# Performance work log

Hardware: AMD Instinct MI355X
Metric: run time of the kernel (lower is better)

Reference implementation:

```python
import jax, jax.numpy as jnp
import numpy as np

B, L, V, D = 512, 41, 4, 64        # batch, seq_len=41 (hard-coded in source), vocab=DNA, d_model=64
NL, DI, N, DTR, K = 3, 128, 16, 4, 4  # n_layer, d_inner=2*D, d_state, dt_rank=ceil(D/16), d_conv
NS = 3  # three parallel stacks (layers1/2/3)


def setup_inputs() -> dict:
    key = jax.random.key(0)
    ks = jax.random.split(key, 16)
    s = 0.02
    nrm = lambda k, sh: jax.random.normal(k, sh, jnp.float32) * s
    A_log = jnp.log(jnp.arange(1, N + 1, dtype=jnp.float32))  # S4D-real init
    return {
        "input_ids": jax.random.randint(ks[0], (B, L), 0, V),
        "embedding": nrm(ks[1], (V, D)),
        # per-stack, per-layer Mamba block params, stacked [NS, NL, ...]
        "in_proj": nrm(ks[2], (NS, NL, D, 2 * DI)),
        "conv_w": nrm(ks[3], (NS, NL, DI, 1, K)),
        "conv_b": jnp.zeros((NS, NL, DI), jnp.float32),
        "x_proj": nrm(ks[4], (NS, NL, DI, DTR + 2 * N)),
        "dt_w": nrm(ks[5], (NS, NL, DTR, DI)),
        "dt_b": jnp.full((NS, NL, DI), -2.0, jnp.float32),
        "A_log": jnp.broadcast_to(A_log, (NS, NL, DI, N)) + 0.0,
        "Dp": jnp.ones((NS, NL, DI), jnp.float32),
        "out_proj": nrm(ks[6], (NS, NL, DI, D)),
        "norm_w": jnp.ones((NS, NL, D), jnp.float32),
        "norm_f_w": jnp.ones((D,), jnp.float32),
        "fusion_w": jnp.zeros((NS,), jnp.float32),  # softmax-weighted fusion of the 3 representations
        # LastDense MLP head: 64*41 -> 384 -> 16 -> 1 (dropout is eval-mode identity)
        "W1": nrm(ks[7], (D * L, 384)), "b1": jnp.zeros((384,), jnp.float32),
        "W2": nrm(ks[8], (384, 16)), "b2": jnp.zeros((16,), jnp.float32),
        "W3": nrm(ks[9], (16, 1)), "b3": jnp.zeros((1,), jnp.float32),
    }


def rmsnorm(x, w, eps=1e-5):
    return x * jax.lax.rsqrt(jnp.mean(x * x, axis=-1, keepdims=True) + eps) * w


def silu(x):
    return x * jax.nn.sigmoid(x)


def mamba_block(x, ip, cw, cb, xp, dw, db, al, dp, op):
    # x: [B, L, D]
    bsz = x.shape[0]
    u, res = jnp.split(x @ ip, 2, axis=-1)  # each [B, L, DI]
    # causal depthwise conv1d (torch padding=3 then [..., :L] == left-pad K-1)
    uc = jax.lax.conv_general_dilated(
        u.transpose(0, 2, 1), cw, window_strides=(1,), padding=[(K - 1, 0)],
        feature_group_count=DI, dimension_numbers=("NCH", "OIH", "NCH"))
    u = silu((uc + cb[None, :, None]).transpose(0, 2, 1))  # [B, L, DI]
    dbl = u @ xp  # [B, L, DTR+2N]
    dt = jax.nn.softplus(dbl[..., :DTR] @ dw + db)           # [B, L, DI]
    Bm = dbl[..., DTR:DTR + N]                               # [B, L, N]
    C = dbl[..., DTR + N:]                                   # [B, L, N]
    A = -jnp.exp(al)                                         # [DI, N]
    dA = jnp.exp(dt[..., None] * A)                          # [B, L, DI, N]
    dBu = dt[..., None] * Bm[:, :, None, :] * u[..., None]   # [B, L, DI, N]

    def step(h, xs):
        dA_t, dBu_t, C_t = xs
        h = dA_t * h + dBu_t                                 # [B, DI, N]
        return h, jnp.einsum("bdn,bn->bd", h, C_t)

    h0 = jnp.zeros((bsz, DI, N), x.dtype)
    _, ys = jax.lax.scan(step, h0, (dA.transpose(1, 0, 2, 3), dBu.transpose(1, 0, 2, 3), C.transpose(1, 0, 2)))
    y = ys.transpose(1, 0, 2) + u * dp                       # [B, L, DI]
    return (y * silu(res)) @ op                              # [B, L, D]


def _forward(input_ids, embedding, in_proj, conv_w, conv_b, x_proj, dt_w, dt_b,
             A_log, Dp, out_proj, norm_w, norm_f_w, fusion_w, W1, b1, W2, b2, W3, b3):
    emb = embedding[input_ids]  # [B, L, D]

    def run_stack(ip, cw, cb, xp, dw, db, al, dp, op, nw):
        x = emb
        for i in range(NL):  # residual: x + MambaBlock(RMSNorm(x))
            x = x + mamba_block(rmsnorm(x, nw[i]), ip[i], cw[i], cb[i], xp[i], dw[i], db[i], al[i], dp[i], op[i])
        return x

    stack_out = jax.vmap(run_stack)(in_proj, conv_w, conv_b, x_proj, dt_w, dt_b,
                                    A_log, Dp, out_proj, norm_w)  # [NS, B, L, D]
    stack_out = rmsnorm(stack_out, norm_f_w)  # final norm_f per stack
    fused = jnp.einsum("s,sbld->bld", jax.nn.softmax(fusion_w), stack_out)  # fusion of 3 reps
    flat = fused.reshape(fused.shape[0], L * D)
    h = jax.nn.relu(flat @ W1 + b1)
    h = jax.nn.relu(h @ W2 + b2)
    logits = (h @ W3 + b3)[:, 0]
    return jax.nn.sigmoid(logits)  # [B]


def reference(input_ids, embedding, in_proj, conv_w, conv_b, x_proj, dt_w, dt_b,
              A_log, Dp, out_proj, norm_w, norm_f_w, fusion_w, W1, b1, W2, b2, W3, b3):
    return _forward(input_ids, embedding, in_proj, conv_w, conv_b, x_proj, dt_w, dt_b,
                    A_log, Dp, out_proj, norm_w, norm_f_w, fusion_w, W1, b1, W2, b2, W3, b3)
```

## Files before the change

kernel.cpp:

```cpp
#include <hip/hip_runtime.h>
#include <hip/hip_bf16.h>
#include <math.h>

#define Bq  512
#define Lq  41
#define Vq  4
#define Dq  64
#define NLq 3
#define DIq 128
#define Nq  16
#define DTRq 4
#define Kq  4
#define NSq 3
#define H1q 384
#define H2q 16
#define FLATq (Lq*Dq)

typedef __attribute__((ext_vector_type(8))) short frag8;
typedef __attribute__((ext_vector_type(4))) float f32x4;

__device__ __forceinline__ float b2f(unsigned short u) {
    union { float f; unsigned int i; } v; v.i = ((unsigned int)u) << 16; return v.f;
}
__device__ __forceinline__ unsigned short f2b(float f) {
    union { float f; unsigned int i; } v; v.f = f;
    unsigned int x = v.i;
    unsigned int r = (x + 0x7fffu + ((x >> 16) & 1u)) >> 16;
    return (unsigned short)r;
}

__global__ __launch_bounds__(256) void init_kernel(const int* __restrict__ ids,
                                                   const float* __restrict__ emb,
                                                   float* __restrict__ X) {
    int idx = blockIdx.x * 256 + threadIdx.x;
    const int total = NSq * Bq * Lq * Dq;
    if (idx < total) {
        int d  = idx & (Dq - 1);
        int t  = idx >> 6;
        int bl = t % (Bq * Lq);
        int id = ids[bl];
        X[idx] = emb[id * Dq + d];
    }
}

__global__ __launch_bounds__(256) void prep_small(const float* __restrict__ in_proj,
                                                  const float* __restrict__ x_proj,
                                                  const float* __restrict__ out_proj,
                                                  unsigned short* __restrict__ Wb_in,
                                                  unsigned short* __restrict__ xp_b,
                                                  unsigned short* __restrict__ op_b) {
    int idx = blockIdx.x * 256 + threadIdx.x;
    if (idx < 9*256*64) {
        int sl = idx >> 14, rem = idx & 16383;
        int n = rem >> 6, k = rem & 63;
        Wb_in[idx] = f2b(in_proj[(size_t)sl*16384 + k*256 + n]);
    } else if (idx < 9*256*64 + 9*48*128) {
        int i2 = idx - 9*256*64;
        int sl = i2 / 6144, rem = i2 % 6144;
        int c = rem >> 7, k = rem & 127;
        float v = (c < 36) ? x_proj[(size_t)sl*(128*36) + k*36 + c] : 0.f;
        xp_b[i2] = f2b(v);
    } else if (idx < 9*256*64 + 9*48*128 + 9*64*128) {
        int i3 = idx - (9*256*64 + 9*48*128);
        int sl = i3 >> 13, rem = i3 & 8191;
        int n = rem >> 7, k = rem & 127;
        op_b[i3] = f2b(out_proj[(size_t)sl*8192 + k*64 + n]);
    }
}

__global__ __launch_bounds__(256) void transpose_w1(const float* __restrict__ W1,
                                                    unsigned short* __restrict__ W1b) {
    __shared__ float t[64][65];
    const int k0 = blockIdx.x * 64, n0 = blockIdx.y * 64;
    for (int idx = threadIdx.x; idx < 4096; idx += 256) {
        int kr = idx >> 6, nc = idx & 63;
        t[kr][nc] = W1[(size_t)(k0 + kr) * H1q + n0 + nc];
    }
    __syncthreads();
    for (int idx = threadIdx.x; idx < 4096; idx += 256) {
        int nr = idx >> 6, kc = idx & 63;
        W1b[(size_t)(n0 + nr) * FLATq + k0 + kc] = f2b(t[kc][nr]);
    }
}

__global__ __launch_bounds__(256, 4) void layer_kernel(
    float* __restrict__ X,
    const unsigned short* __restrict__ Wb_in,
    const float* __restrict__ conv_w,
    const float* __restrict__ conv_b,
    const unsigned short* __restrict__ xp_b,
    const float* __restrict__ dt_w,
    const float* __restrict__ dt_b,
    const float* __restrict__ A_log,
    const float* __restrict__ Dp,
    const unsigned short* __restrict__ op_b,
    const float* __restrict__ norm_w,
    int layer)
{
    const int b = blockIdx.x, s = blockIdx.y, tid = threadIdx.x;
    const int sl = s * NLq + layer;
    const int wave = tid >> 6, lane = tid & 63;
    const int nl = lane & 15, quad = lane >> 4;

    __shared__ unsigned short xn_lb[48][72];
    __shared__ unsigned short u_lb [48][136];
    __shared__ unsigned short rs_lb[41][136];
    __shared__ float dbl_s[41][48];

    float* xrow = X + ((size_t)(s * Bq + b)) * (Lq * Dq);

    {
        const float nwv = norm_w[(size_t)sl * Dq + lane];
        for (int l = wave; l < 48; l += 4) {
            if (l < Lq) {
                float v  = xrow[l * Dq + lane];
                float ss = v * v;
                #pragma unroll
                for (int off = 32; off; off >>= 1) ss += __shfl_xor(ss, off, 64);
                float scale = rsqrtf(ss * (1.0f / Dq) + 1e-5f);
                xn_lb[l][lane] = f2b(v * scale * nwv);
            } else {
                xn_lb[l][lane] = 0;
            }
        }
    }
    __syncthreads();

    {
        #pragma unroll
        for (int t = 0; t < 12; ++t) {
            const int id = wave * 12 + t;
            const int mt = id >> 4, nt = id & 15;
            const unsigned short* Wp = Wb_in + ((size_t)(sl * 256 + nt * 16 + nl)) * 64 + quad * 8;
            frag8 a0 = *(const frag8*)&xn_lb[mt * 16 + nl][quad * 8];
            frag8 a1 = *(const frag8*)&xn_lb[mt * 16 + nl][32 + quad * 8];
            frag8 b0 = *(const frag8*)&Wp[0];
            frag8 b1 = *(const frag8*)&Wp[32];
            f32x4 c = {0.f, 0.f, 0.f, 0.f};
            c = __builtin_amdgcn_mfma_f32_16x16x32_bf16(a0, b0, c, 0, 0, 0);
            c = __builtin_amdgcn_mfma_f32_16x16x32_bf16(a1, b1, c, 0, 0, 0);
            const int col = nt * 16 + nl;
            const int r0 = mt * 16 + quad * 4;
            if (col < DIq) {
                #pragma unroll
                for (int r = 0; r < 4; ++r) u_lb[r0 + r][col] = f2b(c[r]);
            } else {
                const int d = col - DIq;
                #pragma unroll
                for (int r = 0; r < 4; ++r) {
                    int row = r0 + r;
                    if (row < Lq) {
                        float v = c[r];
                        rs_lb[row][d] = f2b(v / (1.f + __expf(-v)));
                    }
                }
            }
        }
    }
    __syncthreads();

    {
        const float* cw = conv_w + (size_t)sl * (DIq * Kq);
        const int d = tid >> 1, half = tid & 1;
        const float c0 = cw[d*4+0], c1 = cw[d*4+1], c2 = cw[d*4+2], c3 = cw[d*4+3];
        const float cbv = conv_b[(size_t)sl * DIq + d];
        float w0 = 0.f, w1 = 0.f, w2 = 0.f;
        if (half) { w0 = b2f(u_lb[18][d]); w1 = b2f(u_lb[19][d]); w2 = b2f(u_lb[20][d]); }
        const int base = half ? 21 : 0;
        const int cnt  = half ? 20 : 21;
        for (int i = 0; i < cnt; ++i) {
            int l = base + i;
            float cur = b2f(u_lb[l][d]);
            float a = fmaf(w0, c0, fmaf(w1, c1, fmaf(w2, c2, fmaf(cur, c3, cbv))));
            u_lb[l][d] = f2b(a / (1.f + __expf(-a)));
            w0 = w1; w1 = w2; w2 = cur;
        }
    }
    __syncthreads();

    {
        for (int t = wave; t < 9; t += 4) {
            const int mt = t / 3, ct = t % 3;
            f32x4 c = {0.f, 0.f, 0.f, 0.f};
            #pragma unroll
            for (int kt = 0; kt < 4; ++kt) {
                frag8 a  = *(const frag8*)&u_lb[mt * 16 + nl][kt * 32 + quad * 8];
                frag8 bb = *(const frag8*)&xp_b[((size_t)(sl * 48 + ct * 16 + nl)) * 128 + kt * 32 + quad * 8];
                c = __builtin_amdgcn_mfma_f32_16x16x32_bf16(a, bb, c, 0, 0, 0);
            }
            const int col = ct * 16 + nl, r0 = mt * 16 + quad * 4;
            #pragma unroll
            for (int r = 0; r < 4; ++r) {
                int row = r0 + r;
                if (row < Lq) dbl_s[row][col] = c[r];
            }
        }
    }
    __syncthreads();

    {
        const int d = tid >> 1, half = tid & 1;
        const float* al = A_log + (size_t)sl * (DIq * Nq) + d * Nq + half * 8;
        float A[8], h[8];
        #pragma unroll
        for (int n = 0; n < 8; ++n) { A[n] = -__expf(al[n]); h[n] = 0.f; }
        const float* dw = dt_w + (size_t)sl * (DTRq * DIq);
        const float dw0 = dw[d], dw1 = dw[DIq + d], dw2 = dw[2*DIq + d], dw3 = dw[3*DIq + d];
        const float dbv = dt_b[(size_t)sl * DIq + d];
        const float dpd = Dp[(size_t)sl * DIq + d];
        for (int l = 0; l < Lq; ++l) {
            float4 q0 = *(const float4*)&dbl_s[l][0];
            float x  = fmaf(q0.x, dw0, fmaf(q0.y, dw1, fmaf(q0.z, dw2, fmaf(q0.w, dw3, dbv))));
            float dt_ = fmaxf(x, 0.f) + __logf(1.f + __expf(-fabsf(x)));
            float u_  = b2f(u_lb[l][d]);
            float rsv = b2f(rs_lb[l][d]);
            float4 B0 = *(const float4*)&dbl_s[l][4  + half * 8];
            float4 B1 = *(const float4*)&dbl_s[l][8  + half * 8];
            float4 C0 = *(const float4*)&dbl_s[l][20 + half * 8];
            float4 C1 = *(const float4*)&dbl_s[l][24 + half * 8];
            float dtu = dt_ * u_;
            float Bv[8] = {B0.x,B0.y,B0.z,B0.w,B1.x,B1.y,B1.z,B1.w};
            float Cv[8] = {C0.x,C0.y,C0.z,C0.w,C1.x,C1.y,C1.z,C1.w};
            float y = 0.f;
            #pragma unroll
            for (int n = 0; n < 8; ++n) {
                float dA = __expf(dt_ * A[n]);
                h[n] = fmaf(dA, h[n], Bv[n] * dtu);
                y    = fmaf(h[n], Cv[n], y);
            }
            y += __shfl_xor(y, 1, 64);
            if (!half) u_lb[l][d] = f2b(fmaf(u_, dpd, y) * rsv);
        }
    }
    __syncthreads();

    {
        const int ntG = wave;
        for (int mt = 0; mt < 3; ++mt) {
            f32x4 c = {0.f, 0.f, 0.f, 0.f};
            #pragma unroll
            for (int kt = 0; kt < 4; ++kt) {
                frag8 a  = *(const frag8*)&u_lb[mt * 16 + nl][kt * 32 + quad * 8];
                frag8 bb = *(const frag8*)&op_b[((size_t)(sl * 64 + ntG * 16 + nl)) * 128 + kt * 32 + quad * 8];
                c = __builtin_amdgcn_mfma_f32_16x16x32_bf16(a, bb, c, 0, 0, 0);
            }
            const int j = ntG * 16 + nl, r0 = mt * 16 + quad * 4;
            #pragma unroll
            for (int r = 0; r < 4; ++r) {
                int row = r0 + r;
                if (row < Lq) xrow[row * Dq + j] += c[r];
            }
        }
    }
}

__global__ __launch_bounds__(256) void head_fuse(const float* __restrict__ X,
                                                 const float* __restrict__ norm_f_w,
                                                 const float* __restrict__ fusion_w,
                                                 unsigned short* __restrict__ Flat_b) {
    const int b    = blockIdx.x;
    const int tid  = threadIdx.x;
    const int wave = tid >> 6, lane = tid & 63;

    float fw0 = fusion_w[0], fw1 = fusion_w[1], fw2 = fusion_w[2];
    float m  = fmaxf(fw0, fmaxf(fw1, fw2));
    float e0 = __expf(fw0 - m), e1 = __expf(fw1 - m), e2 = __expf(fw2 - m);
    float inv = 1.f / (e0 + e1 + e2);
    float w[NSq] = {e0 * inv, e1 * inv, e2 * inv};
    float nf = norm_f_w[lane];

    for (int l = wave; l < Lq; l += 4) {
        float acc = 0.f;
        #pragma unroll
        for (int s = 0; s < NSq; ++s) {
            float v  = X[(((size_t)s * Bq + b) * Lq + l) * Dq + lane];
            float ss = v * v;
            #pragma unroll
            for (int off = 32; off; off >>= 1) ss += __shfl_xor(ss, off, 64);
            acc += w[s] * v * rsqrtf(ss * (1.0f / Dq) + 1e-5f);
        }
        Flat_b[(size_t)b * FLATq + l * Dq + lane] = f2b(acc * nf);
    }
}

__global__ __launch_bounds__(256) void head_gemm1(const unsigned short* __restrict__ Flat_b,
                                                  const unsigned short* __restrict__ W1b,
                                                  float* __restrict__ H1) {
    const int tid = threadIdx.x;
    const int wave = tid >> 6, lane = tid & 63;
    const int nl = lane & 15, quad = lane >> 4;
    const int mt = blockIdx.x;
    const int nt = blockIdx.y * 4 + wave;

    const unsigned short* Arow = Flat_b + (size_t)(mt * 16 + nl) * FLATq + quad * 8;
    const unsigned short* Brow = W1b    + (size_t)(nt * 16 + nl) * FLATq + quad * 8;
    f32x4 c = {0.f, 0.f, 0.f, 0.f};
    #pragma unroll 2
    for (int k0 = 0; k0 < FLATq; k0 += 32) {
        frag8 a  = *(const frag8*)(Arow + k0);
        frag8 bb = *(const frag8*)(Brow + k0);
        c = __builtin_amdgcn_mfma_f32_16x16x32_bf16(a, bb, c, 0, 0, 0);
    }
    #pragma unroll
    for (int r = 0; r < 4; ++r)
        H1[(size_t)(mt * 16 + quad * 4 + r) * H1q + nt * 16 + nl] = c[r];
}

__global__ __launch_bounds__(256) void head_final(const float* __restrict__ H1,
                                                  const float* __restrict__ b1,
                                                  const float* __restrict__ W2,
                                                  const float* __restrict__ b2,
                                                  const float* __restrict__ W3,
                                                  const float* __restrict__ b3,
                                                  float* __restrict__ out) {
    const int b = blockIdx.x, tid = threadIdx.x;
    __shared__ float h1[H1q];
    __shared__ float h2[H2q];
    for (int j = tid; j < H1q; j += 256)
        h1[j] = fmaxf(H1[(size_t)b * H1q + j] + b1[j], 0.f);
    __syncthreads();
    {
        const int g = tid >> 4, t = tid & 15;
        float acc = 0.f;
        for (int k = t; k < H1q; k += 16) acc += h1[k] * W2[k * H2q + g];
        #pragma unroll
        for (int off = 8; off; off >>= 1) acc += __shfl_xor(acc, off, 64);
        if (t == 0) h2[g] = fmaxf(acc + b2[g], 0.f);
    }
    __syncthreads();
    if (tid == 0) {
        float z = b3[0];
        #pragma unroll
        for (int k = 0; k < H2q; ++k) z += h2[k] * W3[k];
        out[b] = 1.f / (1.f + __expf(-z));
    }
}

extern "C" void kernel_launch(void* const* d_in, const int* in_sizes, int n_in,
                              void* d_out, int out_size, void* d_ws, size_t ws_size,
                              hipStream_t stream) {
    const int*   ids      = (const int*)  d_in[0];
    const float* emb      = (const float*)d_in[1];
    const float* in_proj  = (const float*)d_in[2];
    const float* conv_w   = (const float*)d_in[3];
    const float* conv_b   = (const float*)d_in[4];
    const float* x_proj   = (const float*)d_in[5];
    const float* dt_w     = (const float*)d_in[6];
    const float* dt_b     = (const float*)d_in[7];
    const float* A_log    = (const float*)d_in[8];
    const float* Dp       = (const float*)d_in[9];
    const float* out_proj = (const float*)d_in[10];
    const float* norm_w   = (const float*)d_in[11];
    const float* norm_f_w = (const float*)d_in[12];
    const float* fusion_w = (const float*)d_in[13];
    const float* W1       = (const float*)d_in[14];
    const float* b1       = (const float*)d_in[15];
    const float* W2       = (const float*)d_in[16];
    const float* b2       = (const float*)d_in[17];
    const float* W3       = (const float*)d_in[18];
    const float* b3       = (const float*)d_in[19];
    float* out = (float*)d_out;

    float* X = (float*)d_ws;
    unsigned short* Flat_b = (unsigned short*)(X + (size_t)NSq*Bq*Lq*Dq);
    unsigned short* Wb_in  = Flat_b + (size_t)Bq*FLATq;
    unsigned short* xp_b   = Wb_in  + 9*256*64;
    unsigned short* op_b   = xp_b   + 9*48*128;
    unsigned short* W1b    = op_b   + 9*64*128;
    float* H1 = X;

    const int prep_total = 9*256*64 + 9*48*128 + 9*64*128;
    hipLaunchKernelGGL(prep_small, dim3((prep_total + 255) / 256), dim3(256), 0, stream,
                       in_proj, x_proj, out_proj, Wb_in, xp_b, op_b);
    hipLaunchKernelGGL(transpose_w1, dim3(FLATq/64, H1q/64), dim3(256), 0, stream,
                       W1, W1b);

    const int total = NSq * Bq * Lq * Dq;
    hipLaunchKernelGGL(init_kernel, dim3((total + 255) / 256), dim3(256), 0, stream,
                       ids, emb, X);

    for (int layer = 0; layer < NLq; ++layer) {
        hipLaunchKernelGGL(layer_kernel, dim3(Bq, NSq), dim3(256), 0, stream,
                           X, Wb_in, conv_w, conv_b, xp_b, dt_w, dt_b,
                           A_log, Dp, op_b, norm_w, layer);
    }

    hipLaunchKernelGGL(head_fuse, dim3(Bq), dim3(256), 0, stream,
                       X, norm_f_w, fusion_w, Flat_b);

    hipLaunchKernelGGL(head_gemm1, dim3(Bq/16, H1q/64), dim3(256), 0, stream,
                       Flat_b, W1b, H1);

    hipLaunchKernelGGL(head_final, dim3(Bq), dim3(256), 0, stream,
                       H1, b1, W2, b2, W3, b3, out);
}
```

Baseline: 362.9 us.

## Fuse three Mamba layers into one kernel with LDS-resident residual and merged head

Merges the embedding init and all three per-layer launches into a single mamba_stack kernel that keeps the residual stream in LDS across layers and writes X to global only once at the end. It also merges the two prep kernels into one launch and fuses the head GEMM with the MLP tail. Several math shortcuts are added: truncating bf16 conversion, hardware rcp, rsq and exp2, and a dbl_s buffer that aliases the xn buffer to save LDS. These cut launches and global round-trips, but truncation rounding and the fused head (only 32 blocks) may change accuracy and parallelism.

New measurement: 380.2 us. 4.8% more time.

```diff
diff --git a/kernel.cpp b/kernel.cpp
--- a/kernel.cpp
+++ b/kernel.cpp
@@ -22,69 +22,63 @@
 __device__ __forceinline__ float b2f(unsigned short u) {
     union { float f; unsigned int i; } v; v.i = ((unsigned int)u) << 16; return v.f;
 }
-__device__ __forceinline__ unsigned short f2b(float f) {
+__device__ __forceinline__ unsigned short f2b_rne(float f) {
     union { float f; unsigned int i; } v; v.f = f;
     unsigned int x = v.i;
-    unsigned int r = (x + 0x7fffu + ((x >> 16) & 1u)) >> 16;
-    return (unsigned short)r;
-}
-
-__global__ __launch_bounds__(256) void init_kernel(const int* __restrict__ ids,
-                                                   const float* __restrict__ emb,
-                                                   float* __restrict__ X) {
-    int idx = blockIdx.x * 256 + threadIdx.x;
-    const int total = NSq * Bq * Lq * Dq;
-    if (idx < total) {
-        int d  = idx & (Dq - 1);
-        int t  = idx >> 6;
-        int bl = t % (Bq * Lq);
-        int id = ids[bl];
-        X[idx] = emb[id * Dq + d];
-    }
-}
-
-__global__ __launch_bounds__(256) void prep_small(const float* __restrict__ in_proj,
-                                                  const float* __restrict__ x_proj,
-                                                  const float* __restrict__ out_proj,
-                                                  unsigned short* __restrict__ Wb_in,
-                                                  unsigned short* __restrict__ xp_b,
-                                                  unsigned short* __restrict__ op_b) {
-    int idx = blockIdx.x * 256 + threadIdx.x;
+    return (unsigned short)((x + 0x7fffu + ((x >> 16) & 1u)) >> 16);
+}
+__device__ __forceinline__ unsigned short f2b_tr(float f) {
+    union { float f; unsigned int i; } v; v.f = f;
+    return (unsigned short)(v.i >> 16);
+}
+__device__ __forceinline__ float fast_rcp(float x) { return __builtin_amdgcn_rcpf(x); }
+
+__global__ __launch_bounds__(256) void prep_kernel(const float* __restrict__ W1,
+                                                   const float* __restrict__ in_proj,
+                                                   const float* __restrict__ x_proj,
+                                                   const float* __restrict__ out_proj,
+                                                   unsigned short* __restrict__ W1b,
+                                                   unsigned short* __restrict__ Wb_in,
+                                                   unsigned short* __restrict__ xp_b,
+                                                   unsigned short* __restrict__ op_b) {
+    const int bx = blockIdx.x;
+    if (bx < 246) {
+        __shared__ float t[64][65];
+        const int k0 = (bx / 6) * 64, n0 = (bx % 6) * 64;
+        for (int idx = threadIdx.x; idx < 4096; idx += 256) {
+            int kr = idx >> 6, nc = idx & 63;
+            t[kr][nc] = W1[(size_t)(k0 + kr) * H1q + n0 + nc];
+        }
+        __syncthreads();
+        for (int idx = threadIdx.x; idx < 4096; idx += 256) {
+            int nr = idx >> 6, kc = idx & 63;
+            W1b[(size_t)(n0 + nr) * FLATq + k0 + kc] = f2b_rne(t[kc][nr]);
+        }
+        return;
+    }
+    int idx = (bx - 246) * 256 + threadIdx.x;
     if (idx < 9*256*64) {
         int sl = idx >> 14, rem = idx & 16383;
         int n = rem >> 6, k = rem & 63;
-        Wb_in[idx] = f2b(in_proj[(size_t)sl*16384 + k*256 + n]);
+        Wb_in[idx] = f2b_rne(in_proj[(size_t)sl*16384 + k*256 + n]);
     } else if (idx < 9*256*64 + 9*48*128) {
         int i2 = idx - 9*256*64;
         int sl = i2 / 6144, rem = i2 % 6144;
         int c = rem >> 7, k = rem & 127;
         float v = (c < 36) ? x_proj[(size_t)sl*(128*36) + k*36 + c] : 0.f;
-        xp_b[i2] = f2b(v);
+        xp_b[i2] = f2b_rne(v);
     } else if (idx < 9*256*64 + 9*48*128 + 9*64*128) {
         int i3 = idx - (9*256*64 + 9*48*128);
         int sl = i3 >> 13, rem = i3 & 8191;
         int n = rem >> 7, k = rem & 127;
-        op_b[i3] = f2b(out_proj[(size_t)sl*8192 + k*64 + n]);
-    }
-}
-
-__global__ __launch_bounds__(256) void transpose_w1(const float* __restrict__ W1,
-                                                    unsigned short* __restrict__ W1b) {
-    __shared__ float t[64][65];
-    const int k0 = blockIdx.x * 64, n0 = blockIdx.y * 64;
-    for (int idx = threadIdx.x; idx < 4096; idx += 256) {
-        int kr = idx >> 6, nc = idx & 63;
-        t[kr][nc] = W1[(size_t)(k0 + kr) * H1q + n0 + nc];
-    }
-    __syncthreads();
-    for (int idx = threadIdx.x; idx < 4096; idx += 256) {
-        int nr = idx >> 6, kc = idx & 63;
-        W1b[(size_t)(n0 + nr) * FLATq + k0 + kc] = f2b(t[kc][nr]);
-    }
-}
-
-__global__ __launch_bounds__(256, 4) void layer_kernel(
+        op_b[i3] = f2b_rne(out_proj[(size_t)sl*8192 + k*64 + n]);
+    }
+}
+
+__global__ __launch_bounds__(256, 4) void mamba_stack(
     float* __restrict__ X,
+    const int* __restrict__ ids,
+    const float* __restrict__ emb,
     const unsigned short* __restrict__ Wb_in,
     const float* __restrict__ conv_w,
     const float* __restrict__ conv_b,
@@ -94,163 +88,182 @@
     const float* __restrict__ A_log,
     const float* __restrict__ Dp,
     const unsigned short* __restrict__ op_b,
-    const float* __restrict__ norm_w,
-    int layer)
+    const float* __restrict__ norm_w)
 {
     const int b = blockIdx.x, s = blockIdx.y, tid = threadIdx.x;
-    const int sl = s * NLq + layer;
     const int wave = tid >> 6, lane = tid & 63;
     const int nl = lane & 15, quad = lane >> 4;
 
-    __shared__ unsigned short xn_lb[48][72];
-    __shared__ unsigned short u_lb [48][136];
-    __shared__ unsigned short rs_lb[41][136];
-    __shared__ float dbl_s[41][48];
-
-    float* xrow = X + ((size_t)(s * Bq + b)) * (Lq * Dq);
-
-    {
-        const float nwv = norm_w[(size_t)sl * Dq + lane];
-        for (int l = wave; l < 48; l += 4) {
-            if (l < Lq) {
-                float v  = xrow[l * Dq + lane];
-                float ss = v * v;
+    __shared__ float          xt  [Lq][64];
+    __shared__ unsigned short u_lb[48][136];
+    __shared__ unsigned short rs_lb[Lq][128];
+    __shared__ __align__(16) char un_buf[6912];
+    unsigned short (*xn_lb)[72] = (unsigned short(*)[72])un_buf;
+    float          (*dbl_s)[40] = (float(*)[40])un_buf;
+
+    for (int l = wave; l < Lq; l += 4) {
+        int id = ids[b * Lq + l];
+        xt[l][lane] = emb[id * Dq + lane];
+    }
+
+    for (int layer = 0; layer < NLq; ++layer) {
+        const int sl = s * NLq + layer;
+
+        {
+            const float nwv = norm_w[(size_t)sl * Dq + lane];
+            for (int l = wave; l < 48; l += 4) {
+                if (l < Lq) {
+                    float v  = xt[l][lane];
+                    float ss = v * v;
+                    #pragma unroll
+                    for (int off = 32; off; off >>= 1) ss += __shfl_xor(ss, off, 64);
+                    float scale = __builtin_amdgcn_rsqf(ss * (1.0f / Dq) + 1e-5f);
+                    xn_lb[l][lane] = f2b_tr(v * scale * nwv);
+                } else {
+                    xn_lb[l][lane] = 0;
+                }
+            }
+        }
+        __syncthreads();
+
+        {
+            #pragma unroll
+            for (int t = 0; t < 12; ++t) {
+                const int id = wave * 12 + t;
+                const int mt = id >> 4, nt = id & 15;
+                const unsigned short* Wp = Wb_in + ((size_t)(sl * 256 + nt * 16 + nl)) * 64 + quad * 8;
+                frag8 a0 = *(const frag8*)&xn_lb[mt * 16 + nl][quad * 8];
+                frag8 a1 = *(const frag8*)&xn_lb[mt * 16 + nl][32 + quad * 8];
+                frag8 b0 = *(const frag8*)&Wp[0];
+                frag8 b1 = *(const frag8*)&Wp[32];
+                f32x4 c = {0.f, 0.f, 0.f, 0.f};
+                c = __builtin_amdgcn_mfma_f32_16x16x32_bf16(a0, b0, c, 0, 0, 0);
+                c = __builtin_amdgcn_mfma_f32_16x16x32_bf16(a1, b1, c, 0, 0, 0);
+                const int col = nt * 16 + nl;
+                const int r0 = mt * 16 + quad * 4;
+                if (col < DIq) {
+                    #pragma unroll
+                    for (int r = 0; r < 4; ++r) u_lb[r0 + r][col] = f2b_tr(c[r]);
+                } else {
+                    const int d = col - DIq;
+                    #pragma unroll
+                    for (int r = 0; r < 4; ++r) {
+                        int row = r0 + r;
+                        if (row < Lq) {
+                            float v = c[r];
+                            rs_lb[row][d] = f2b_tr(v * fast_rcp(1.f + __expf(-v)));
+                        }
+                    }
+                }
+            }
+        }
+        __syncthreads();
+
+        {
+            const float* cw = conv_w + (size_t)sl * (DIq * Kq);
+            const int d = tid >> 1, half = tid & 1;
+            const float c0 = cw[d*4+0], c1 = cw[d*4+1], c2 = cw[d*4+2], c3 = cw[d*4+3];
+            const float cbv = conv_b[(size_t)sl * DIq + d];
+            float w0 = 0.f, w1 = 0.f, w2 = 0.f;
+            if (half) { w0 = b2f(u_lb[18][d]); w1 = b2f(u_lb[19][d]); w2 = b2f(u_lb[20][d]); }
+            const int base = half ? 21 : 0;
+            const int cnt  = half ? 20 : 21;
+            for (int i = 0; i < cnt; ++i) {
+                int l = base + i;
+                float cur = b2f(u_lb[l][d]);
+                float a = fmaf(w0, c0, fmaf(w1, c1, fmaf(w2, c2, fmaf(cur, c3, cbv))));
+                u_lb[l][d] = f2b_tr(a * fast_rcp(1.f + __expf(-a)));
+                w0 = w1; w1 = w2; w2 = cur;
+            }
+        }
+        __syncthreads();
+
+        {
+            for (int t = wave; t < 9; t += 4) {
+                const int mt = t / 3, ct = t % 3;
+                f32x4 c = {0.f, 0.f, 0.f, 0.f};
                 #pragma unroll
-                for (int off = 32; off; off >>= 1) ss += __shfl_xor(ss, off, 64);
-                float scale = rsqrtf(ss * (1.0f / Dq) + 1e-5f);
-                xn_lb[l][lane] = f2b(v * scale * nwv);
-            } else {
-                xn_lb[l][lane] = 0;
-            }
-        }
-    }
-    __syncthreads();
-
-    {
-        #pragma unroll
-        for (int t = 0; t < 12; ++t) {
-            const int id = wave * 12 + t;
-            const int mt = id >> 4, nt = id & 15;
-            const unsigned short* Wp = Wb_in + ((size_t)(sl * 256 + nt * 16 + nl)) * 64 + quad * 8;
-            frag8 a0 = *(const frag8*)&xn_lb[mt * 16 + nl][quad * 8];
-            frag8 a1 = *(const frag8*)&xn_lb[mt * 16 + nl][32 + quad * 8];
-            frag8 b0 = *(const frag8*)&Wp[0];
-            frag8 b1 = *(const frag8*)&Wp[32];
-            f32x4 c = {0.f, 0.f, 0.f, 0.f};
-            c = __builtin_amdgcn_mfma_f32_16x16x32_bf16(a0, b0, c, 0, 0, 0);
-            c = __builtin_amdgcn_mfma_f32_16x16x32_bf16(a1, b1, c, 0, 0, 0);
-            const int col = nt * 16 + nl;
-            const int r0 = mt * 16 + quad * 4;
-            if (col < DIq) {
+                for (int kt = 0; kt < 4; ++kt) {
+                    frag8 a  = *(const frag8*)&u_lb[mt * 16 + nl][kt * 32 + quad * 8];
+                    frag8 bb = *(const frag8*)&xp_b[((size_t)(sl * 48 + ct * 16 + nl)) * 128 + kt * 32 + quad * 8];
+                    c = __builtin_amdgcn_mfma_f32_16x16x32_bf16(a, bb, c, 0, 0, 0);
+                }
+                const int col = ct * 16 + nl, r0 = mt * 16 + quad * 4;
+                if (col < 40) {
+                    #pragma unroll
+                    for (int r = 0; r < 4; ++r) {
+                        int row = r0 + r;
+                        if (row < Lq) dbl_s[row][col] = c[r];
+                    }
+                }
+            }
+        }
+        __syncthreads();
+
+        {
+            const int d = tid >> 1, half = tid & 1;
+            const float* al = A_log + (size_t)sl * (DIq * Nq) + d * Nq + half * 8;
+            float A2[8], h[8];
+            #pragma unroll
+            for (int n = 0; n < 8; ++n) {
+                A2[n] = -__expf(al[n]) * 1.442695041f;
+                h[n] = 0.f;
+            }
+            const float* dw = dt_w + (size_t)sl * (DTRq * DIq);
+            const float dw0 = dw[d], dw1 = dw[DIq + d], dw2 = dw[2*DIq + d], dw3 = dw[3*DIq + d];
+            const float dbv = dt_b[(size_t)sl * DIq + d];
+            const float dpd = Dp[(size_t)sl * DIq + d];
+            for (int l = 0; l < Lq; ++l) {
+                float4 q0 = *(const float4*)&dbl_s[l][0];
+                float x  = fmaf(q0.x, dw0, fmaf(q0.y, dw1, fmaf(q0.z, dw2, fmaf(q0.w, dw3, dbv))));
+                float dt_ = fmaxf(x, 0.f) + __logf(1.f + __expf(-fabsf(x)));
+                float u_  = b2f(u_lb[l][d]);
+                float rsv = b2f(rs_lb[l][d]);
+                float4 B0 = *(const float4*)&dbl_s[l][4  + half * 8];
+                float4 B1 = *(const float4*)&dbl_s[l][8  + half * 8];
+                float4 C0 = *(const float4*)&dbl_s[l][20 + half * 8];
+                float4 C1 = *(const float4*)&dbl_s[l][24 + half * 8];
+                float dtu = dt_ * u_;
+                float Bv[8] = {B0.x,B0.y,B0.z,B0.w,B1.x,B1.y,B1.z,B1.w};
+                float Cv[8] = {C0.x,C0.y,C0.z,C0.w,C1.x,C1.y,C1.z,C1.w};
+                float y = 0.f;
                 #pragma unroll
-                for (int r = 0; r < 4; ++r) u_lb[r0 + r][col] = f2b(c[r]);
-            } else {
-                const int d = col - DIq;
+                for (int n = 0; n < 8; ++n) {
+                    float dA = __builtin_amdgcn_exp2f(dt_ * A2[n]);
+                    h[n] = fmaf(dA, h[n], Bv[n] * dtu);
+                    y    = fmaf(h[n], Cv[n], y);
+                }
+                y += __shfl_xor(y, 1, 64);
+                if (!half) u_lb[l][d] = f2b_tr(fmaf(u_, dpd, y) * rsv);
+            }
+        }
+        __syncthreads();
+
+        {
+            const int ntG = wave;
+            for (int mt = 0; mt < 3; ++mt) {
+                f32x4 c = {0.f, 0.f, 0.f, 0.f};
+                #pragma unroll
+                for (int kt = 0; kt < 4; ++kt) {
+                    frag8 a  = *(const frag8*)&u_lb[mt * 16 + nl][kt * 32 + quad * 8];
+                    frag8 bb = *(const frag8*)&op_b[((size_t)(sl * 64 + ntG * 16 + nl)) * 128 + kt * 32 + quad * 8];
+                    c = __builtin_amdgcn_mfma_f32_16x16x32_bf16(a, bb, c, 0, 0, 0);
+                }
+                const int j = ntG * 16 + nl, r0 = mt * 16 + quad * 4;
                 #pragma unroll
                 for (int r = 0; r < 4; ++r) {
                     int row = r0 + r;
-                    if (row < Lq) {
-                        float v = c[r];
-                        rs_lb[row][d] = f2b(v / (1.f + __expf(-v)));
-                    }
-                }
-            }
-        }
-    }
-    __syncthreads();
+                    if (row < Lq) xt[row][j] += c[r];
+                }
+            }
+        }
+        __syncthreads();
+    }
 
     {
-        const float* cw = conv_w + (size_t)sl * (DIq * Kq);
-        const int d = tid >> 1, half = tid & 1;
-        const float c0 = cw[d*4+0], c1 = cw[d*4+1], c2 = cw[d*4+2], c3 = cw[d*4+3];
-        const float cbv = conv_b[(size_t)sl * DIq + d];
-        float w0 = 0.f, w1 = 0.f, w2 = 0.f;
-        if (half) { w0 = b2f(u_lb[18][d]); w1 = b2f(u_lb[19][d]); w2 = b2f(u_lb[20][d]); }
-        const int base = half ? 21 : 0;
-        const int cnt  = half ? 20 : 21;
-        for (int i = 0; i < cnt; ++i) {
-            int l = base + i;
-            float cur = b2f(u_lb[l][d]);
-            float a = fmaf(w0, c0, fmaf(w1, c1, fmaf(w2, c2, fmaf(cur, c3, cbv))));
-            u_lb[l][d] = f2b(a / (1.f + __expf(-a)));
-            w0 = w1; w1 = w2; w2 = cur;
-        }
-    }
-    __syncthreads();
-
-    {
-        for (int t = wave; t < 9; t += 4) {
-            const int mt = t / 3, ct = t % 3;
-            f32x4 c = {0.f, 0.f, 0.f, 0.f};
-            #pragma unroll
-            for (int kt = 0; kt < 4; ++kt) {
-                frag8 a  = *(const frag8*)&u_lb[mt * 16 + nl][kt * 32 + quad * 8];
-                frag8 bb = *(const frag8*)&xp_b[((size_t)(sl * 48 + ct * 16 + nl)) * 128 + kt * 32 + quad * 8];
-                c = __builtin_amdgcn_mfma_f32_16x16x32_bf16(a, bb, c, 0, 0, 0);
-            }
-            const int col = ct * 16 + nl, r0 = mt * 16 + quad * 4;
-            #pragma unroll
-            for (int r = 0; r < 4; ++r) {
-                int row = r0 + r;
-                if (row < Lq) dbl_s[row][col] = c[r];
-            }
-        }
-    }
-    __syncthreads();
-
-    {
-        const int d = tid >> 1, half = tid & 1;
-        const float* al = A_log + (size_t)sl * (DIq * Nq) + d * Nq + half * 8;
-        float A[8], h[8];
-        #pragma unroll
-        for (int n = 0; n < 8; ++n) { A[n] = -__expf(al[n]); h[n] = 0.f; }
-        const float* dw = dt_w + (size_t)sl * (DTRq * DIq);
-        const float dw0 = dw[d], dw1 = dw[DIq + d], dw2 = dw[2*DIq + d], dw3 = dw[3*DIq + d];
-        const float dbv = dt_b[(size_t)sl * DIq + d];
-        const float dpd = Dp[(size_t)sl * DIq + d];
-        for (int l = 0; l < Lq; ++l) {
-            float4 q0 = *(const float4*)&dbl_s[l][0];
-            float x  = fmaf(q0.x, dw0, fmaf(q0.y, dw1, fmaf(q0.z, dw2, fmaf(q0.w, dw3, dbv))));
-            float dt_ = fmaxf(x, 0.f) + __logf(1.f + __expf(-fabsf(x)));
-            float u_  = b2f(u_lb[l][d]);
-            float rsv = b2f(rs_lb[l][d]);
-            float4 B0 = *(const float4*)&dbl_s[l][4  + half * 8];
-            float4 B1 = *(const float4*)&dbl_s[l][8  + half * 8];
-            float4 C0 = *(const float4*)&dbl_s[l][20 + half * 8];
-            float4 C1 = *(const float4*)&dbl_s[l][24 + half * 8];
-            float dtu = dt_ * u_;
-            float Bv[8] = {B0.x,B0.y,B0.z,B0.w,B1.x,B1.y,B1.z,B1.w};
-            float Cv[8] = {C0.x,C0.y,C0.z,C0.w,C1.x,C1.y,C1.z,C1.w};
-            float y = 0.f;
-            #pragma unroll
-            for (int n = 0; n < 8; ++n) {
-                float dA = __expf(dt_ * A[n]);
-                h[n] = fmaf(dA, h[n], Bv[n] * dtu);
-                y    = fmaf(h[n], Cv[n], y);
-            }
-            y += __shfl_xor(y, 1, 64);
-            if (!half) u_lb[l][d] = f2b(fmaf(u_, dpd, y) * rsv);
-        }
-    }
-    __syncthreads();
-
-    {
-        const int ntG = wave;
-        for (int mt = 0; mt < 3; ++mt) {
-            f32x4 c = {0.f, 0.f, 0.f, 0.f};
-            #pragma unroll
-            for (int kt = 0; kt < 4; ++kt) {
-                frag8 a  = *(const frag8*)&u_lb[mt * 16 + nl][kt * 32 + quad * 8];
-                frag8 bb = *(const frag8*)&op_b[((size_t)(sl * 64 + ntG * 16 + nl)) * 128 + kt * 32 + quad * 8];
-                c = __builtin_amdgcn_mfma_f32_16x16x32_bf16(a, bb, c, 0, 0, 0);
-            }
-            const int j = ntG * 16 + nl, r0 = mt * 16 + quad * 4;
-            #pragma unroll
-            for (int r = 0; r < 4; ++r) {
-                int row = r0 + r;
-                if (row < Lq) xrow[row * Dq + j] += c[r];
-            }
-        }
+        float* xrow = X + ((size_t)(s * Bq + b)) * (Lq * Dq);
+        const float* xf = &xt[0][0];
+        for (int idx = tid; idx < Lq * Dq; idx += 256) xrow[idx] = xf[idx];
     }
 }
 
@@ -265,7 +278,7 @@
     float fw0 = fusion_w[0], fw1 = fusion_w[1], fw2 = fusion_w[2];
     float m  = fmaxf(fw0, fmaxf(fw1, fw2));
     float e0 = __expf(fw0 - m), e1 = __expf(fw1 - m), e2 = __expf(fw2 - m);
-    float inv = 1.f / (e0 + e1 + e2);
+    float inv = fast_rcp(e0 + e1 + e2);
     float w[NSq] = {e0 * inv, e1 * inv, e2 * inv};
     float nf = norm_f_w[lane];
 
@@ -277,62 +290,63 @@
             float ss = v * v;
             #pragma unroll
             for (int off = 32; off; off >>= 1) ss += __shfl_xor(ss, off, 64);
-            acc += w[s] * v * rsqrtf(ss * (1.0f / Dq) + 1e-5f);
-        }
-        Flat_b[(size_t)b * FLATq + l * Dq + lane] = f2b(acc * nf);
-    }
-}
-
-__global__ __launch_bounds__(256) void head_gemm1(const unsigned short* __restrict__ Flat_b,
-                                                  const unsigned short* __restrict__ W1b,
-                                                  float* __restrict__ H1) {
+            acc += w[s] * v * __builtin_amdgcn_rsqf(ss * (1.0f / Dq) + 1e-5f);
+        }
+        Flat_b[(size_t)b * FLATq + l * Dq + lane] = f2b_tr(acc * nf);
+    }
+}
+
+__global__ __launch_bounds__(256) void head_tail(const unsigned short* __restrict__ Flat_b,
+                                                 const unsigned short* __restrict__ W1b,
+                                                 const float* __restrict__ b1,
+                                                 const float* __restrict__ W2,
+                                                 const float* __restrict__ b2,
+                                                 const float* __restrict__ W3,
+                                                 const float* __restrict__ b3,
+                                                 float* __restrict__ out) {
     const int tid = threadIdx.x;
     const int wave = tid >> 6, lane = tid & 63;
     const int nl = lane & 15, quad = lane >> 4;
-    const int mt = blockIdx.x;
-    const int nt = blockIdx.y * 4 + wave;
-
-    const unsigned short* Arow = Flat_b + (size_t)(mt * 16 + nl) * FLATq + quad * 8;
-    const unsigned short* Brow = W1b    + (size_t)(nt * 16 + nl) * FLATq + quad * 8;
-    f32x4 c = {0.f, 0.f, 0.f, 0.f};
-    #pragma unroll 2
-    for (int k0 = 0; k0 < FLATq; k0 += 32) {
-        frag8 a  = *(const frag8*)(Arow + k0);
-        frag8 bb = *(const frag8*)(Brow + k0);
-        c = __builtin_amdgcn_mfma_f32_16x16x32_bf16(a, bb, c, 0, 0, 0);
-    }
+    const int b0 = blockIdx.x * 16;
+
+    __shared__ float H1s[16][388];
+    __shared__ float h2s[16][16];
+
+    const unsigned short* Arow = Flat_b + (size_t)(b0 + nl) * FLATq + quad * 8;
     #pragma unroll
-    for (int r = 0; r < 4; ++r)
-        H1[(size_t)(mt * 16 + quad * 4 + r) * H1q + nt * 16 + nl] = c[r];
-}
-
-__global__ __launch_bounds__(256) void head_final(const float* __restrict__ H1,
-                                                  const float* __restrict__ b1,
-                                                  const float* __restrict__ W2,
-                                                  const float* __restrict__ b2,
-                                                  const float* __restrict__ W3,
-                                                  const float* __restrict__ b3,
-                                                  float* __restrict__ out) {
-    const int b = blockIdx.x, tid = threadIdx.x;
-    __shared__ float h1[H1q];
-    __shared__ float h2[H2q];
-    for (int j = tid; j < H1q; j += 256)
-        h1[j] = fmaxf(H1[(size_t)b * H1q + j] + b1[j], 0.f);
+    for (int t = 0; t < 3; ++t) {
+        const int ntA = wave + 4 * t, ntB = ntA + 12;
+        const unsigned short* BrA = W1b + (size_t)(ntA * 16 + nl) * FLATq + quad * 8;
+        const unsigned short* BrB = W1b + (size_t)(ntB * 16 + nl) * FLATq + quad * 8;
+        f32x4 ca = {0.f,0.f,0.f,0.f}, cb = {0.f,0.f,0.f,0.f};
+        for (int k0 = 0; k0 < FLATq; k0 += 32) {
+            frag8 a  = *(const frag8*)(Arow + k0);
+            frag8 ba = *(const frag8*)(BrA + k0);
+            frag8 bbv = *(const frag8*)(BrB + k0);
+            ca = __builtin_amdgcn_mfma_f32_16x16x32_bf16(a, ba, ca, 0, 0, 0);
+            cb = __builtin_amdgcn_mfma_f32_16x16x32_bf16(a, bbv, cb, 0, 0, 0);
+        }
+        #pragma unroll
+        for (int r = 0; r < 4; ++r) {
+            int row = quad * 4 + r;
+            int colA = ntA * 16 + nl, colB = ntB * 16 + nl;
+            H1s[row][colA] = fmaxf(ca[r] + b1[colA], 0.f);
+            H1s[row][colB] = fmaxf(cb[r] + b1[colB], 0.f);
+        }
+    }
     __syncthreads();
     {
-        const int g = tid >> 4, t = tid & 15;
-        float acc = 0.f;
-        for (int k = t; k < H1q; k += 16) acc += h1[k] * W2[k * H2q + g];
-        #pragma unroll
-        for (int off = 8; off; off >>= 1) acc += __shfl_xor(acc, off, 64);
-        if (t == 0) h2[g] = fmaxf(acc + b2[g], 0.f);
+        const int row = tid >> 4, g = tid & 15;
+        float acc = b2[g];
+        for (int k = 0; k < H1q; ++k) acc = fmaf(H1s[row][k], W2[k * H2q + g], acc);
+        h2s[row][g] = fmaxf(acc, 0.f);
     }
     __syncthreads();
-    if (tid == 0) {
+    if (tid < 16) {
         float z = b3[0];
         #pragma unroll
-        for (int k = 0; k < H2q; ++k) z += h2[k] * W3[k];
-        out[b] = 1.f / (1.f + __expf(-z));
+        for (int k = 0; k < H2q; ++k) z = fmaf(h2s[tid][k], W3[k], z);
+        out[b0 + tid] = fast_rcp(1.f + __expf(-z));
     }
 }
 
@@ -367,30 +381,17 @@
     unsigned short* xp_b   = Wb_in  + 9*256*64;
     unsigned short* op_b   = xp_b   + 9*48*128;
     unsigned short* W1b    = op_b   + 9*64*128;
-    float* H1 = X;
-
-    const int prep_total = 9*256*64 + 9*48*128 + 9*64*128;
-    hipLaunchKernelGGL(prep_small, dim3((prep_total + 255) / 256), dim3(256), 0, stream,
-                       in_proj, x_proj, out_proj, Wb_in, xp_b, op_b);
-    hipLaunchKernelGGL(transpose_w1, dim3(FLATq/64, H1q/64), dim3(256), 0, stream,
-                       W1, W1b);
-
-    const int total = NSq * Bq * Lq * Dq;
-    hipLaunchKernelGGL(init_kernel, dim3((total + 255) / 256), dim3(256), 0, stream,
-                       ids, emb, X);
-
-    for (int layer = 0; layer < NLq; ++layer) {
-        hipLaunchKernelGGL(layer_kernel, dim3(Bq, NSq), dim3(256), 0, stream,
-                           X, Wb_in, conv_w, conv_b, xp_b, dt_w, dt_b,
-                           A_log, Dp, op_b, norm_w, layer);
-    }
+
+    hipLaunchKernelGGL(prep_kernel, dim3(246 + 1080), dim3(256), 0, stream,
+                       W1, in_proj, x_proj, out_proj, W1b, Wb_in, xp_b, op_b);
+
+    hipLaunchKernelGGL(mamba_stack, dim3(Bq, NSq), dim3(256), 0, stream,
+                       X, ids, emb, Wb_in, conv_w, conv_b, xp_b, dt_w, dt_b,
+                       A_log, Dp, op_b, norm_w);
 
     hipLaunchKernelGGL(head_fuse, dim3(Bq), dim3(256), 0, stream,
                        X, norm_f_w, fusion_w, Flat_b);
 
-    hipLaunchKernelGGL(head_gemm1, dim3(Bq/16, H1q/64), dim3(256), 0, stream,
-                       Flat_b, W1b, H1);
-
-    hipLaunchKernelGGL(head_final, dim3(Bq), dim3(256), 0, stream,
-                       H1, b1, W2, b2, W3, b3, out);
-}
+    hipLaunchKernelGGL(head_tail, dim3(Bq/16), dim3(256), 0, stream,
+                       Flat_b, W1b, b1, W2, b2, W3, b3, out);
+}
```
